# Kernel optimization log

Measured on AMD Instinct MI355X. Metric: run time of the kernel, lower is better.

Reference implementation:

```python
import jax, jax.numpy as jnp
import numpy as np

NUM_HEADS = 16


def setup_inputs() -> dict:
    key = jax.random.key(0)
    ks = jax.random.split(key, 6)
    B, S, D = 2, 2048, 2048
    scale = 0.02
    return {
        "hidden_states": jax.random.normal(ks[0], (B, S, D), dtype=jnp.float32),
        "Wq": jax.random.normal(ks[1], (D, D), dtype=jnp.float32) * scale,
        "Wk": jax.random.normal(ks[2], (D, D), dtype=jnp.float32) * scale,
        "Wv": jax.random.normal(ks[3], (D, D), dtype=jnp.float32) * scale,
        "Wo": jax.random.normal(ks[4], (D, D), dtype=jnp.float32) * scale,
        "bo": jnp.zeros((D,), dtype=jnp.float32),
    }


def reference(hidden_states, Wq, Wk, Wv, Wo, bo):
    B, S, D = hidden_states.shape
    H = NUM_HEADS
    hd = D // H

    def split_heads(t):  # [B,S,D] -> [B,H,S,hd]
        return t.reshape(B, S, H, hd).transpose(0, 2, 1, 3)

    q = split_heads(hidden_states @ Wq)
    k = split_heads(hidden_states @ Wk)
    v = split_heads(hidden_states @ Wv)

    # Note: GPT-Neo does NOT scale by 1/sqrt(head_dim); scores computed in fp32.
    scores = jnp.einsum("bhqd,bhkd->bhqk", q.astype(jnp.float32), k.astype(jnp.float32))
    causal = jnp.tril(jnp.ones((S, S), dtype=bool))  # [S,S], True = attend
    mask_value = jnp.finfo(jnp.float32).min
    scores = jnp.where(causal[None, None, :, :], scores, mask_value)
    attn = jax.nn.softmax(scores, axis=-1).astype(v.dtype)

    ctx = jnp.einsum("bhqk,bhkd->bhqd", attn, v)  # [B,H,S,hd]
    ctx = ctx.transpose(0, 2, 1, 3).reshape(B, S, D)  # merge heads
    out = ctx @ Wo + bo
    return out
```

## Files before the change

### kernel.cpp

```cpp
#include <hip/hip_runtime.h>
#include <hip/hip_bf16.h>
#include <math.h>

#define BATCH 2
#define SEQ   2048
#define DDIM  2048
#define NH    16
#define HD    128
#define MROWS (BATCH * SEQ)

typedef unsigned short u16;
typedef __bf16 bf16x8 __attribute__((ext_vector_type(8)));
typedef float  f32x4  __attribute__((ext_vector_type(4)));

__device__ __forceinline__ u16 f2bf(float f) {
  unsigned int u = __float_as_uint(f);
  u += 0x7fffu + ((u >> 16) & 1u);
  return (u16)(u >> 16);
}
__device__ __forceinline__ float bf2f(u16 h) {
  return __uint_as_float(((unsigned int)h) << 16);
}

__device__ __forceinline__ void gload16(const void* g, void* s) {
  __builtin_amdgcn_global_load_lds((const __attribute__((address_space(1))) void*)g,
                                   (__attribute__((address_space(3))) void*)s, 16, 0, 0);
}

__global__ void split_x(const float* __restrict__ in, u16* __restrict__ hi,
                        u16* __restrict__ lo) {
  const int i = blockIdx.x * blockDim.x + threadIdx.x;
  float4 v = ((const float4*)in)[i];
  ushort4 h, l;
  h.x = f2bf(v.x); l.x = f2bf(v.x - bf2f(h.x));
  h.y = f2bf(v.y); l.y = f2bf(v.y - bf2f(h.y));
  h.z = f2bf(v.z); l.z = f2bf(v.z - bf2f(h.z));
  h.w = f2bf(v.w); l.w = f2bf(v.w - bf2f(h.w));
  ((ushort4*)hi)[i] = h;
  ((ushort4*)lo)[i] = l;
}

__global__ void transpose_w(const float* __restrict__ W, u16* __restrict__ Wth,
                            u16* __restrict__ Wtl) {
  __shared__ float t[32][33];
  const int tx = threadIdx.x, ty = threadIdx.y;
  const int c0 = blockIdx.x * 32, r0 = blockIdx.y * 32;
#pragma unroll
  for (int i = 0; i < 4; ++i)
    t[ty + i * 8][tx] = W[(size_t)(r0 + ty + i * 8) * DDIM + c0 + tx];
  __syncthreads();
#pragma unroll
  for (int i = 0; i < 4; ++i) {
    const float v = t[tx][ty + i * 8];
    const u16 h = f2bf(v);
    const size_t idx = (size_t)(c0 + ty + i * 8) * DDIM + r0 + tx;
    Wth[idx] = h;
    if (Wtl) Wtl[idx] = f2bf(v - bf2f(h));
  }
}

__global__ void transpose_v(const u16* __restrict__ V, u16* __restrict__ Vt) {
  __shared__ u16 t[32][33];
  const int tx = threadIdx.x, ty = threadIdx.y;
  const int s0 = blockIdx.x * 32;
  const int d0 = blockIdx.y * 32;
  const int bh = blockIdx.z;
  const int b = bh >> 4, h = bh & 15;
#pragma unroll
  for (int i = 0; i < 4; ++i)
    t[ty + i * 8][tx] = V[(size_t)(b * SEQ + s0 + ty + i * 8) * DDIM + h * HD + d0 + tx];
  __syncthreads();
#pragma unroll
  for (int i = 0; i < 4; ++i)
    Vt[((size_t)bh * HD + d0 + ty + i * 8) * SEQ + s0 + tx] = t[tx][ty + i * 8];
}

template <int MODE>
__global__ __launch_bounds__(256)
void gemm_kernel(const u16* __restrict__ A, const u16* __restrict__ Bt,
                 void* __restrict__ Cout, const float* __restrict__ bias) {
  constexpr int K = DDIM, N = DDIM;
  __shared__ __align__(16) u16 As[128 * 64];
  __shared__ __align__(16) u16 Bs[128 * 64];
  const int tid = threadIdx.x;
  const int wave = tid >> 6;
  const int lane = tid & 63;
  const int lr = lane & 15, lg = lane >> 4;
  const int bm = blockIdx.y * 128, bn = blockIdx.x * 128;
  const int wr = wave >> 1, wc = wave & 1;

  f32x4 acc[4][4] = {};

  const int srow = wave * 32 + (lane >> 3);
  const int scol = (lane & 7) * 8;
  const u16* Ag = A  + (size_t)(bm + srow) * K + scol;
  const u16* Bg = Bt + (size_t)(bn + srow) * K + scol;

  for (int k0 = 0; k0 < K; k0 += 64) {
    __syncthreads();
#pragma unroll
    for (int it = 0; it < 4; ++it) {
      gload16(Ag + (size_t)it * 8 * K + k0, &As[(wave * 32 + it * 8) * 64]);
      gload16(Bg + (size_t)it * 8 * K + k0, &Bs[(wave * 32 + it * 8) * 64]);
    }
    __syncthreads();
#pragma unroll
    for (int kk = 0; kk < 64; kk += 32) {
      bf16x8 af[4], bfr[4];
#pragma unroll
      for (int i = 0; i < 4; ++i)
        af[i] = *(const bf16x8*)&As[(wr * 64 + i * 16 + lr) * 64 + kk + lg * 8];
#pragma unroll
      for (int j = 0; j < 4; ++j)
        bfr[j] = *(const bf16x8*)&Bs[(wc * 64 + j * 16 + lr) * 64 + kk + lg * 8];
#pragma unroll
      for (int i = 0; i < 4; ++i)
#pragma unroll
        for (int j = 0; j < 4; ++j)
          acc[i][j] = __builtin_amdgcn_mfma_f32_16x16x32_bf16(af[i], bfr[j], acc[i][j], 0, 0, 0);
    }
  }

#pragma unroll
  for (int i = 0; i < 4; ++i) {
    const int row0 = bm + wr * 64 + i * 16 + lg * 4;
#pragma unroll
    for (int j = 0; j < 4; ++j) {
      const int col = bn + wc * 64 + j * 16 + lr;
#pragma unroll
      for (int e = 0; e < 4; ++e) {
        const int row = row0 + e;
        const float v = acc[i][j][e];
        if constexpr (MODE == 0) {
          ((u16*)Cout)[(size_t)row * N + col] = f2bf(v);
        } else {
          ((float*)Cout)[(size_t)row * N + col] = v + bias[col];
        }
      }
    }
  }
}

template <int TERMS, bool WRITE_LO>
__global__ __launch_bounds__(256)
void gemm3_kernel(const u16* __restrict__ Ah, const u16* __restrict__ Al,
                  const u16* __restrict__ Bh, const u16* __restrict__ Bl,
                  u16* __restrict__ Ch, u16* __restrict__ Cl) {
  constexpr int K = DDIM, N = DDIM;
  __shared__ __align__(16) u16 Ash[128 * 64];
  __shared__ __align__(16) u16 Asl[TERMS == 3 ? 128 * 64 : 8];
  __shared__ __align__(16) u16 Bsh[128 * 64];
  __shared__ __align__(16) u16 Bsl[128 * 64];
  const int tid = threadIdx.x;
  const int wave = tid >> 6;
  const int lane = tid & 63;
  const int lr = lane & 15, lg = lane >> 4;
  const int bm = blockIdx.y * 128, bn = blockIdx.x * 128;
  const int wr = wave >> 1, wc = wave & 1;

  f32x4 acc[4][4] = {};

  const int srow = wave * 32 + (lane >> 3);
  const int scol = (lane & 7) * 8;
  const size_t aoff = (size_t)(bm + srow) * K + scol;
  const size_t boff = (size_t)(bn + srow) * K + scol;

  for (int k0 = 0; k0 < K; k0 += 64) {
    __syncthreads();
#pragma unroll
    for (int it = 0; it < 4; ++it) {
      const size_t ro = (size_t)it * 8 * K + k0;
      const int ls = (wave * 32 + it * 8) * 64;
      gload16(Ah + aoff + ro, &Ash[ls]);
      if constexpr (TERMS == 3) gload16(Al + aoff + ro, &Asl[ls]);
      gload16(Bh + boff + ro, &Bsh[ls]);
      gload16(Bl + boff + ro, &Bsl[ls]);
    }
    __syncthreads();
#pragma unroll
    for (int kk = 0; kk < 64; kk += 32) {
      bf16x8 ah[4], al[4], bh[4], bl[4];
#pragma unroll
      for (int i = 0; i < 4; ++i) {
        const int off = (wr * 64 + i * 16 + lr) * 64 + kk + lg * 8;
        ah[i] = *(const bf16x8*)&Ash[off];
        if constexpr (TERMS == 3) al[i] = *(const bf16x8*)&Asl[off];
      }
#pragma unroll
      for (int j = 0; j < 4; ++j) {
        const int off = (wc * 64 + j * 16 + lr) * 64 + kk + lg * 8;
        bh[j] = *(const bf16x8*)&Bsh[off];
        bl[j] = *(const bf16x8*)&Bsl[off];
      }
#pragma unroll
      for (int i = 0; i < 4; ++i)
#pragma unroll
        for (int j = 0; j < 4; ++j) {
          acc[i][j] = __builtin_amdgcn_mfma_f32_16x16x32_bf16(ah[i], bh[j], acc[i][j], 0, 0, 0);
          acc[i][j] = __builtin_amdgcn_mfma_f32_16x16x32_bf16(ah[i], bl[j], acc[i][j], 0, 0, 0);
          if constexpr (TERMS == 3)
            acc[i][j] = __builtin_amdgcn_mfma_f32_16x16x32_bf16(al[i], bh[j], acc[i][j], 0, 0, 0);
        }
    }
  }

#pragma unroll
  for (int i = 0; i < 4; ++i) {
    const int row0 = bm + wr * 64 + i * 16 + lg * 4;
#pragma unroll
    for (int j = 0; j < 4; ++j) {
      const int col = bn + wc * 64 + j * 16 + lr;
#pragma unroll
      for (int e = 0; e < 4; ++e) {
        const float v = acc[i][j][e];
        const u16 h = f2bf(v);
        const size_t idx = (size_t)(row0 + e) * N + col;
        Ch[idx] = h;
        if constexpr (WRITE_LO) Cl[idx] = f2bf(v - bf2f(h));
      }
    }
  }
}

__global__ __launch_bounds__(512, 1)
void attn_kernel(const u16* __restrict__ Qh, const u16* __restrict__ Khp,
                 const u16* __restrict__ Klp, const u16* __restrict__ Vt,
                 u16* __restrict__ ctx) {
  __shared__ __align__(16) u16 Ksh[2][64 * 128];
  __shared__ __align__(16) u16 Ksl[2][64 * 128];
  __shared__ __align__(16) u16 Vs [2][128 * 64];
  __shared__ __align__(16) u16 P_lds[8][16 * 32];
  const int tid = threadIdx.x;
  const int wave = tid >> 6, lane = tid & 63;
  const int lr = lane & 15, lg = lane >> 4;

  const int id = blockIdx.y * 16 + blockIdx.x;
  const int xcd = id & 7;
  const int j = id >> 3;
  int bh, qb;
  if (j < 32) { bh = xcd * 4 + (j >> 4);            qb = 15 - (j & 15); }
  else        { const int jj = j - 32;
                bh = xcd * 4 + 2 + (jj >> 4);       qb = jj & 15; }
  const int q0 = qb * 128;
  const int b = bh >> 4, h = bh & 15;
  const int qw = q0 + wave * 16;
  const float NEG_INF = -__builtin_inff();

  const u16* Kg = Khp + (size_t)b * SEQ * DDIM + h * HD;
  const u16* Lg = Klp + (size_t)b * SEQ * DDIM + h * HD;
  const u16* Vg = Vt + (size_t)bh * HD * SEQ;

  bf16x8 qf[4];
#pragma unroll
  for (int kk = 0; kk < 4; ++kk)
    qf[kk] = *(const bf16x8*)&Qh[(size_t)(b * SEQ + qw + lr) * DDIM + h * HD + kk * 32 + lg * 8];

  bf16x8 ones;
#pragma unroll
  for (int i = 0; i < 8; ++i) ones[i] = (__bf16)1.0f;

  const int krow0 = wave * 4 + (lane >> 4);
  const int kcolb = (lane & 15) << 4;
  const int vrow0 = wave * 8 + (lane >> 3);
  const int vcolb = (lane & 7) << 4;

  auto STAGE = [&](int buf, int t) {
    const int kbase = t * 64;
#pragma unroll
    for (int it = 0; it < 2; ++it) {
      const int r = it * 32 + krow0;
      const int c = (kcolb ^ ((r & 7) << 4)) >> 1;
      const size_t g = (size_t)(kbase + r) * DDIM + c;
      gload16(Kg + g, &Ksh[buf][it * 4096 + wave * 512]);
      gload16(Lg + g, &Ksl[buf][it * 4096 + wave * 512]);
    }
#pragma unroll
    for (int it = 0; it < 2; ++it) {
      const int d = it * 64 + vrow0;
      const int c = (vcolb ^ ((d & 7) << 4)) >> 1;
      gload16(Vg + (size_t)d * SEQ + kbase + c, &Vs[buf][it * 4096 + wave * 512]);
    }
  };

  float m[4];
  f32x4 lsum = {};
#pragma unroll
  for (int e = 0; e < 4; ++e) m[e] = NEG_INF;
  f32x4 o[8] = {};

  const int nt = 2 * qb + 2;
  int cur = 0;
  STAGE(0, 0);
  __syncthreads();

  for (int t = 0; t < nt; ++t) {
    if (t + 1 < nt) STAGE(cur ^ 1, t + 1);
#pragma unroll
    for (int ks = 0; ks < 2; ++ks) {
      const int k0 = t * 64 + ks * 32;
      if (k0 <= qw + 15) {
        f32x4 s[2] = {};
        __builtin_amdgcn_s_setprio(1);
#pragma unroll
        for (int fc = 0; fc < 2; ++fc) {
          const int r = ks * 32 + fc * 16 + lr;
          const int sw = (r & 7) << 4;
#pragma unroll
          for (int kk = 0; kk < 4; ++kk) {
            const int idx = r * 128 + (((kk * 64 + lg * 16) ^ sw) >> 1);
            bf16x8 kfh = *(const bf16x8*)&Ksh[cur][idx];
            bf16x8 kfl = *(const bf16x8*)&Ksl[cur][idx];
            s[fc] = __builtin_amdgcn_mfma_f32_16x16x32_bf16(qf[kk], kfh, s[fc], 0, 0, 0);
            s[fc] = __builtin_amdgcn_mfma_f32_16x16x32_bf16(qf[kk], kfl, s[fc], 0, 0, 0);
          }
        }
        __builtin_amdgcn_s_setprio(0);
        if (k0 + 31 > qw) {
#pragma unroll
          for (int e = 0; e < 4; ++e) {
            const int row = qw + lg * 4 + e;
#pragma unroll
            for (int fc = 0; fc < 2; ++fc) {
              const int key = k0 + fc * 16 + lr;
              if (key > row) s[fc][e] = NEG_INF;
            }
          }
        }
        float rm[4];
#pragma unroll
        for (int e = 0; e < 4; ++e) {
          float r0 = fmaxf(s[0][e], s[1][e]);
          r0 = fmaxf(r0, __shfl_xor(r0, 1));
          r0 = fmaxf(r0, __shfl_xor(r0, 2));
          r0 = fmaxf(r0, __shfl_xor(r0, 4));
          r0 = fmaxf(r0, __shfl_xor(r0, 8));
          rm[e] = r0;
        }
        const float need = fmaxf(fmaxf(rm[0] - m[0], rm[1] - m[1]),
                                 fmaxf(rm[2] - m[2], rm[3] - m[3]));
        if (!__all(need <= 8.0f)) {
#pragma unroll
          for (int e = 0; e < 4; ++e) {
            const float mn = fmaxf(m[e], rm[e]);
            const float al = __expf(m[e] - mn);
#pragma unroll
            for (int db = 0; db < 8; ++db) o[db][e] *= al;
            lsum[e] *= al;
            m[e] = mn;
          }
        }
#pragma unroll
        for (int e = 0; e < 4; ++e) {
          const float p0 = __expf(s[0][e] - m[e]);
          const float p1 = __expf(s[1][e] - m[e]);
          const int q = lg * 4 + e;
          const int sw = (q & 3) << 4;
          P_lds[wave][q * 32 + ((((lr) * 2) ^ sw) >> 1)] = f2bf(p0);
          P_lds[wave][q * 32 + ((((16 + lr) * 2) ^ sw) >> 1)] = f2bf(p1);
        }
        __builtin_amdgcn_wave_barrier();
        bf16x8 pf = *(const bf16x8*)&P_lds[wave][lr * 32 + (((lg * 16) ^ ((lr & 3) << 4)) >> 1)];
        __builtin_amdgcn_wave_barrier();
        __builtin_amdgcn_s_setprio(1);
#pragma unroll
        for (int db = 0; db < 8; ++db) {
          const int d = db * 16 + lr;
          const int idx = d * 64 + (((ks * 64 + lg * 16) ^ ((d & 7) << 4)) >> 1);
          bf16x8 vf = *(const bf16x8*)&Vs[cur][idx];
          o[db] = __builtin_amdgcn_mfma_f32_16x16x32_bf16(pf, vf, o[db], 0, 0, 0);
        }
        lsum = __builtin_amdgcn_mfma_f32_16x16x32_bf16(pf, ones, lsum, 0, 0, 0);
        __builtin_amdgcn_s_setprio(0);
      }
    }
    __syncthreads();
    cur ^= 1;
  }

#pragma unroll
  for (int db = 0; db < 8; ++db)
#pragma unroll
    for (int e = 0; e < 4; ++e) {
      const float v = o[db][e] / lsum[e];
      ctx[(size_t)(b * SEQ + qw + lg * 4 + e) * DDIM + h * HD + db * 16 + lr] = f2bf(v);
    }
}

extern "C" void kernel_launch(void* const* d_in, const int* in_sizes, int n_in,
                              void* d_out, int out_size, void* d_ws, size_t ws_size,
                              hipStream_t stream) {
  const float* X  = (const float*)d_in[0];
  const float* Wq = (const float*)d_in[1];
  const float* Wk = (const float*)d_in[2];
  const float* Wv = (const float*)d_in[3];
  const float* Wo = (const float*)d_in[4];
  const float* bo = (const float*)d_in[5];
  float* out = (float*)d_out;

  const size_t SZ_XD = (size_t)MROWS * DDIM * 2;
  const size_t SZ_W  = (size_t)DDIM * DDIM * 2;

  char* p = (char*)d_ws;
  auto alloc = [&](size_t bytes) {
    char* r = p;
    p += (bytes + 255) & ~(size_t)255;
    return r;
  };
  u16* Xh  = (u16*)alloc(SZ_XD);
  u16* Xl  = (u16*)alloc(SZ_XD);
  u16* Wbh = (u16*)alloc(SZ_W);
  u16* Wbl = (u16*)alloc(SZ_W);
  u16* Qh  = (u16*)alloc(SZ_XD);
  u16* Kh  = (u16*)alloc(SZ_XD);
  u16* Kl  = (u16*)alloc(SZ_XD);
  u16* Vb  = (u16*)alloc(SZ_XD);
  u16* Vt  = Xh;
  u16* ctx = Qh;

  split_x<<<(MROWS * DDIM) / 1024, 256, 0, stream>>>(X, Xh, Xl);

  dim3 tb(32, 8);
  dim3 gg(DDIM / 128, MROWS / 128);

  transpose_w<<<dim3(64, 64), tb, 0, stream>>>(Wq, Wbh, Wbl);
  gemm3_kernel<2, false><<<gg, 256, 0, stream>>>(Xh, Xl, Wbh, Wbl, Qh, nullptr);

  transpose_w<<<dim3(64, 64), tb, 0, stream>>>(Wk, Wbh, Wbl);
  gemm3_kernel<3, true><<<gg, 256, 0, stream>>>(Xh, Xl, Wbh, Wbl, Kh, Kl);

  transpose_w<<<dim3(64, 64), tb, 0, stream>>>(Wv, Wbh, nullptr);
  gemm_kernel<0><<<gg, 256, 0, stream>>>(Xh, Wbh, Vb, nullptr);

  transpose_v<<<dim3(SEQ / 32, HD / 32, BATCH * NH), tb, 0, stream>>>(Vb, Vt);

  transpose_w<<<dim3(64, 64), tb, 0, stream>>>(Wo, Wbh, nullptr);

  attn_kernel<<<dim3(16, 32), 512, 0, stream>>>(Qh, Kh, Kl, Vt, ctx);

  gemm_kernel<2><<<gg, 256, 0, stream>>>(ctx, Wbh, out, bo);
}
```

Before: 593.3 us.

## Restructure attention around 32x32x16 MFMA with register-resident P

Rewrites the flash-attention kernel to use 32x32x16 bf16 MFMAs, with 4 waves of 32 query rows each instead of 8 waves of 16 rows. The softmax probabilities are packed and exchanged between half-waves with shuffles rather than round-tripped through LDS. The row sum is now accumulated with scalar adds instead of an extra MFMA against a ones vector. The output is staged through LDS so ctx can be written as coalesced 16-byte stores. The aim is fewer MFMA issues, fewer LDS accesses and less cross-lane reduction, at the cost of more registers per wave, half as many waves per block, and a simpler block-to-work mapping that may load-balance the causal work differently.

```diff
diff --git a/kernel.cpp b/kernel.cpp
--- a/kernel.cpp
+++ b/kernel.cpp
@@ -12,6 +12,7 @@
 typedef unsigned short u16;
 typedef __bf16 bf16x8 __attribute__((ext_vector_type(8)));
 typedef float  f32x4  __attribute__((ext_vector_type(4)));
+typedef float  f32x16 __attribute__((ext_vector_type(16)));
 
 __device__ __forceinline__ u16 f2bf(float f) {
   unsigned int u = __float_as_uint(f);
@@ -222,42 +223,36 @@
   }
 }
 
-__global__ __launch_bounds__(512, 1)
+__global__ __launch_bounds__(256, 1)
 void attn_kernel(const u16* __restrict__ Qh, const u16* __restrict__ Khp,
                  const u16* __restrict__ Klp, const u16* __restrict__ Vt,
                  u16* __restrict__ ctx) {
   __shared__ __align__(16) u16 Ksh[2][64 * 128];
   __shared__ __align__(16) u16 Ksl[2][64 * 128];
   __shared__ __align__(16) u16 Vs [2][128 * 64];
-  __shared__ __align__(16) u16 P_lds[8][16 * 32];
   const int tid = threadIdx.x;
   const int wave = tid >> 6, lane = tid & 63;
-  const int lr = lane & 15, lg = lane >> 4;
-
-  const int id = blockIdx.y * 16 + blockIdx.x;
+  const int lq = lane & 31;
+  const int hi = lane >> 5;
+  const float NEG_INF = -__builtin_inff();
+
+  const int id = blockIdx.x;
   const int xcd = id & 7;
   const int j = id >> 3;
-  int bh, qb;
-  if (j < 32) { bh = xcd * 4 + (j >> 4);            qb = 15 - (j & 15); }
-  else        { const int jj = j - 32;
-                bh = xcd * 4 + 2 + (jj >> 4);       qb = jj & 15; }
+  const int bh = xcd * 4 + (j >> 4);
+  const int qb = 15 - (j & 15);
   const int q0 = qb * 128;
   const int b = bh >> 4, h = bh & 15;
-  const int qw = q0 + wave * 16;
-  const float NEG_INF = -__builtin_inff();
+  const int qw0 = q0 + wave * 32;
 
   const u16* Kg = Khp + (size_t)b * SEQ * DDIM + h * HD;
   const u16* Lg = Klp + (size_t)b * SEQ * DDIM + h * HD;
   const u16* Vg = Vt + (size_t)bh * HD * SEQ;
 
-  bf16x8 qf[4];
-#pragma unroll
-  for (int kk = 0; kk < 4; ++kk)
-    qf[kk] = *(const bf16x8*)&Qh[(size_t)(b * SEQ + qw + lr) * DDIM + h * HD + kk * 32 + lg * 8];
-
-  bf16x8 ones;
-#pragma unroll
-  for (int i = 0; i < 8; ++i) ones[i] = (__bf16)1.0f;
+  bf16x8 qf[8];
+#pragma unroll
+  for (int ks = 0; ks < 8; ++ks)
+    qf[ks] = *(const bf16x8*)&Qh[(size_t)(b * SEQ + qw0 + lq) * DDIM + h * HD + ks * 16 + hi * 8];
 
   const int krow0 = wave * 4 + (lane >> 4);
   const int kcolb = (lane & 15) << 4;
@@ -267,26 +262,23 @@
   auto STAGE = [&](int buf, int t) {
     const int kbase = t * 64;
 #pragma unroll
-    for (int it = 0; it < 2; ++it) {
-      const int r = it * 32 + krow0;
+    for (int it = 0; it < 4; ++it) {
+      const int r = it * 16 + krow0;
       const int c = (kcolb ^ ((r & 7) << 4)) >> 1;
       const size_t g = (size_t)(kbase + r) * DDIM + c;
-      gload16(Kg + g, &Ksh[buf][it * 4096 + wave * 512]);
-      gload16(Lg + g, &Ksl[buf][it * 4096 + wave * 512]);
-    }
-#pragma unroll
-    for (int it = 0; it < 2; ++it) {
-      const int d = it * 64 + vrow0;
+      gload16(Kg + g, &Ksh[buf][(it * 16 + wave * 4) * 128]);
+      gload16(Lg + g, &Ksl[buf][(it * 16 + wave * 4) * 128]);
+    }
+#pragma unroll
+    for (int it = 0; it < 4; ++it) {
+      const int d = it * 32 + vrow0;
       const int c = (vcolb ^ ((d & 7) << 4)) >> 1;
-      gload16(Vg + (size_t)d * SEQ + kbase + c, &Vs[buf][it * 4096 + wave * 512]);
+      gload16(Vg + (size_t)d * SEQ + kbase + c, &Vs[buf][(it * 32 + wave * 8) * 64]);
     }
   };
 
-  float m[4];
-  f32x4 lsum = {};
-#pragma unroll
-  for (int e = 0; e < 4; ++e) m[e] = NEG_INF;
-  f32x4 o[8] = {};
+  float m = NEG_INF, l = 0.f;
+  f32x16 o[4] = {};
 
   const int nt = 2 * qb + 2;
   int cur = 0;
@@ -296,80 +288,70 @@
   for (int t = 0; t < nt; ++t) {
     if (t + 1 < nt) STAGE(cur ^ 1, t + 1);
 #pragma unroll
-    for (int ks = 0; ks < 2; ++ks) {
-      const int k0 = t * 64 + ks * 32;
-      if (k0 <= qw + 15) {
-        f32x4 s[2] = {};
+    for (int ks2 = 0; ks2 < 2; ++ks2) {
+      const int k0 = t * 64 + ks2 * 32;
+      if (k0 <= qw0 + 31) {
+        f32x16 s = {};
         __builtin_amdgcn_s_setprio(1);
 #pragma unroll
-        for (int fc = 0; fc < 2; ++fc) {
-          const int r = ks * 32 + fc * 16 + lr;
-          const int sw = (r & 7) << 4;
-#pragma unroll
-          for (int kk = 0; kk < 4; ++kk) {
-            const int idx = r * 128 + (((kk * 64 + lg * 16) ^ sw) >> 1);
-            bf16x8 kfh = *(const bf16x8*)&Ksh[cur][idx];
-            bf16x8 kfl = *(const bf16x8*)&Ksl[cur][idx];
-            s[fc] = __builtin_amdgcn_mfma_f32_16x16x32_bf16(qf[kk], kfh, s[fc], 0, 0, 0);
-            s[fc] = __builtin_amdgcn_mfma_f32_16x16x32_bf16(qf[kk], kfl, s[fc], 0, 0, 0);
+        for (int d8 = 0; d8 < 8; ++d8) {
+          const int krow = ks2 * 32 + lq;
+          const int cb = ((d8 * 32 + hi * 16) ^ ((krow & 7) << 4)) >> 1;
+          bf16x8 kfh = *(const bf16x8*)&Ksh[cur][krow * 128 + cb];
+          s = __builtin_amdgcn_mfma_f32_32x32x16_bf16(kfh, qf[d8], s, 0, 0, 0);
+          bf16x8 kfl = *(const bf16x8*)&Ksl[cur][krow * 128 + cb];
+          s = __builtin_amdgcn_mfma_f32_32x32x16_bf16(kfl, qf[d8], s, 0, 0, 0);
+        }
+        __builtin_amdgcn_s_setprio(0);
+        if (k0 + 31 > qw0) {
+          const int qrow = qw0 + lq;
+#pragma unroll
+          for (int r = 0; r < 16; ++r) {
+            const int key = k0 + (r & 3) + 8 * (r >> 2) + 4 * hi;
+            if (key > qrow) s[r] = NEG_INF;
           }
         }
-        __builtin_amdgcn_s_setprio(0);
-        if (k0 + 31 > qw) {
-#pragma unroll
-          for (int e = 0; e < 4; ++e) {
-            const int row = qw + lg * 4 + e;
-#pragma unroll
-            for (int fc = 0; fc < 2; ++fc) {
-              const int key = k0 + fc * 16 + lr;
-              if (key > row) s[fc][e] = NEG_INF;
-            }
+        float rm = s[0];
+#pragma unroll
+        for (int r = 1; r < 16; ++r) rm = fmaxf(rm, s[r]);
+        rm = fmaxf(rm, __shfl_xor(rm, 32));
+        if (!__all(rm - m <= 8.0f)) {
+          const float mn = fmaxf(m, rm);
+          const float al = __expf(m - mn);
+#pragma unroll
+          for (int db = 0; db < 4; ++db)
+#pragma unroll
+            for (int r = 0; r < 16; ++r) o[db][r] *= al;
+          l *= al;
+          m = mn;
+        }
+        float ps[16];
+        float ls = 0.f;
+#pragma unroll
+        for (int r = 0; r < 16; ++r) { ps[r] = __expf(s[r] - m); ls += ps[r]; }
+        l += ls + __shfl_xor(ls, 32);
+        unsigned pk[8], sw[8];
+#pragma unroll
+        for (int jj = 0; jj < 8; ++jj) {
+          pk[jj] = (unsigned)f2bf(ps[2 * jj]) | ((unsigned)f2bf(ps[2 * jj + 1]) << 16);
+          sw[jj] = __shfl_xor(pk[jj], 32);
+        }
+        __builtin_amdgcn_s_setprio(1);
+#pragma unroll
+        for (int ksl = 0; ksl < 2; ++ksl) {
+          union { unsigned u[4]; bf16x8 v; } pb;
+          pb.u[0] = hi ? sw[4 * ksl + 2] : pk[4 * ksl + 0];
+          pb.u[1] = hi ? sw[4 * ksl + 3] : pk[4 * ksl + 1];
+          pb.u[2] = hi ? pk[4 * ksl + 2] : sw[4 * ksl + 0];
+          pb.u[3] = hi ? pk[4 * ksl + 3] : sw[4 * ksl + 1];
+#pragma unroll
+          for (int db = 0; db < 4; ++db) {
+            const int d = db * 32 + lq;
+            const int cb = ((ks2 * 64 + ksl * 32 + hi * 16) ^ ((d & 7) << 4)) >> 1;
+            bf16x8 vf = *(const bf16x8*)&Vs[cur][d * 64 + cb];
+            o[db] = __builtin_amdgcn_mfma_f32_32x32x16_bf16(vf, pb.v, o[db], 0, 0, 0);
           }
         }
-        float rm[4];
-#pragma unroll
-        for (int e = 0; e < 4; ++e) {
-          float r0 = fmaxf(s[0][e], s[1][e]);
-          r0 = fmaxf(r0, __shfl_xor(r0, 1));
-          r0 = fmaxf(r0, __shfl_xor(r0, 2));
-          r0 = fmaxf(r0, __shfl_xor(r0, 4));
-          r0 = fmaxf(r0, __shfl_xor(r0, 8));
-          rm[e] = r0;
-        }
-        const float need = fmaxf(fmaxf(rm[0] - m[0], rm[1] - m[1]),
-                                 fmaxf(rm[2] - m[2], rm[3] - m[3]));
-        if (!__all(need <= 8.0f)) {
-#pragma unroll
-          for (int e = 0; e < 4; ++e) {
-            const float mn = fmaxf(m[e], rm[e]);
-            const float al = __expf(m[e] - mn);
-#pragma unroll
-            for (int db = 0; db < 8; ++db) o[db][e] *= al;
-            lsum[e] *= al;
-            m[e] = mn;
-          }
-        }
-#pragma unroll
-        for (int e = 0; e < 4; ++e) {
-          const float p0 = __expf(s[0][e] - m[e]);
-          const float p1 = __expf(s[1][e] - m[e]);
-          const int q = lg * 4 + e;
-          const int sw = (q & 3) << 4;
-          P_lds[wave][q * 32 + ((((lr) * 2) ^ sw) >> 1)] = f2bf(p0);
-          P_lds[wave][q * 32 + ((((16 + lr) * 2) ^ sw) >> 1)] = f2bf(p1);
-        }
-        __builtin_amdgcn_wave_barrier();
-        bf16x8 pf = *(const bf16x8*)&P_lds[wave][lr * 32 + (((lg * 16) ^ ((lr & 3) << 4)) >> 1)];
-        __builtin_amdgcn_wave_barrier();
-        __builtin_amdgcn_s_setprio(1);
-#pragma unroll
-        for (int db = 0; db < 8; ++db) {
-          const int d = db * 16 + lr;
-          const int idx = d * 64 + (((ks * 64 + lg * 16) ^ ((d & 7) << 4)) >> 1);
-          bf16x8 vf = *(const bf16x8*)&Vs[cur][idx];
-          o[db] = __builtin_amdgcn_mfma_f32_16x16x32_bf16(pf, vf, o[db], 0, 0, 0);
-        }
-        lsum = __builtin_amdgcn_mfma_f32_16x16x32_bf16(pf, ones, lsum, 0, 0, 0);
         __builtin_amdgcn_s_setprio(0);
       }
     }
@@ -377,13 +359,27 @@
     cur ^= 1;
   }
 
-#pragma unroll
-  for (int db = 0; db < 8; ++db)
-#pragma unroll
-    for (int e = 0; e < 4; ++e) {
-      const float v = o[db][e] / lsum[e];
-      ctx[(size_t)(b * SEQ + qw + lg * 4 + e) * DDIM + h * HD + db * 16 + lr] = f2bf(v);
-    }
+  u16* sm = (u16*)&Vs[0][0] + wave * 4096;
+#pragma unroll
+  for (int db = 0; db < 4; ++db)
+#pragma unroll
+    for (int jj = 0; jj < 8; ++jj) {
+      const int d0 = db * 32 + 8 * (jj >> 1) + 4 * hi + 2 * (jj & 1);
+      const unsigned w = (unsigned)f2bf(o[db][2 * jj] / l) |
+                         ((unsigned)f2bf(o[db][2 * jj + 1] / l) << 16);
+      *(unsigned*)&sm[((lq * 256 + d0 * 2) ^ ((lq & 7) << 4)) >> 1] = w;
+    }
+  __builtin_amdgcn_wave_barrier();
+  {
+    const int qr = lane >> 1, hb = lane & 1;
+    const size_t rowbase = (size_t)(b * SEQ + qw0 + qr) * DDIM + h * HD + hb * 64;
+#pragma unroll
+    for (int c = 0; c < 8; ++c) {
+      const int byte = (qr * 256 + hb * 128 + c * 16) ^ ((qr & 7) << 4);
+      bf16x8 vv = *(const bf16x8*)&sm[byte >> 1];
+      *(bf16x8*)&ctx[rowbase + c * 8] = vv;
+    }
+  }
 }
 
 extern "C" void kernel_launch(void* const* d_in, const int* in_sizes, int n_in,
@@ -435,7 +431,7 @@
 
   transpose_w<<<dim3(64, 64), tb, 0, stream>>>(Wo, Wbh, nullptr);
 
-  attn_kernel<<<dim3(16, 32), 512, 0, stream>>>(Qh, Kh, Kl, Vt, ctx);
+  attn_kernel<<<512, 256, 0, stream>>>(Qh, Kh, Kl, Vt, ctx);
 
   gemm_kernel<2><<<gg, 256, 0, stream>>>(ctx, Wbh, out, bo);
 }
```

New measurement: 597.5 us. No clear change (+0.7%).
